# Optimization experiments

Hardware: AMD Instinct MI355X
Metric: run time of the kernel (lower is better)

## Reference

```python
import jax, jax.numpy as jnp
import numpy as np
from jax import lax
from jax.scipy.special import logsumexp

B, T, N = 256, 512, 128


def setup_inputs() -> dict:
    key = jax.random.key(0)
    k1, k2, k3 = jax.random.split(key, 3)
    emissions = jax.random.normal(k1, (B, T, N), dtype=jnp.float32)
    tag_ids = jax.random.randint(k2, (B, T), 0, N, dtype=jnp.int64)
    mask = jnp.ones((B, T), dtype=jnp.int32)
    # learned transition matrix (glorot-uniform-ish init)
    limit = float(np.sqrt(6.0 / (N + N)))
    trans = jax.random.uniform(k3, (N, N), minval=-limit, maxval=limit, dtype=jnp.float32)
    return {"emissions": emissions, "tag_ids": tag_ids, "mask": mask, "trans": trans}


def _sequence_score(emissions, tag_ids, maskf, trans):
    # unary: emission score of the gold tag at each valid step
    unary = jnp.take_along_axis(emissions, tag_ids[:, :, None], axis=2)[..., 0]  # [B,T]
    unary = jnp.sum(unary * maskf, axis=1)
    # binary: transition score between consecutive gold tags
    binary = trans[tag_ids[:, :-1], tag_ids[:, 1:]] * maskf[:, 1:]  # [B,T-1]
    return unary + jnp.sum(binary, axis=1)


def _log_norm(emissions, maskf, trans):
    # forward algorithm over time via lax.scan; alpha: [B,N]
    alpha0 = emissions[:, 0]
    em = jnp.swapaxes(emissions, 0, 1)[1:]   # [T-1,B,N]
    mk = jnp.swapaxes(maskf, 0, 1)[1:]       # [T-1,B]

    def step(alpha, xs):
        emit_t, m_t = xs
        new = logsumexp(alpha[:, :, None] + trans[None], axis=1) + emit_t
        alpha = jnp.where(m_t[:, None] > 0, new, alpha)
        return alpha, None

    alpha, _ = lax.scan(step, alpha0, (em, mk))
    return logsumexp(alpha, axis=1)  # [B]


def _viterbi_decode(emissions, maskf, trans):
    alpha0 = emissions[:, 0]
    em = jnp.swapaxes(emissions, 0, 1)[1:]
    mk = jnp.swapaxes(maskf, 0, 1)[1:]
    idx = jnp.arange(N, dtype=jnp.int32)[None]

    def fwd(alpha, xs):
        emit_t, m_t = xs
        scores = alpha[:, :, None] + trans[None]        # [B,N,N]
        bp = jnp.argmax(scores, axis=1).astype(jnp.int32)  # [B,N]
        new = jnp.max(scores, axis=1) + emit_t
        valid = m_t[:, None] > 0
        alpha = jnp.where(valid, new, alpha)
        bp = jnp.where(valid, bp, idx)  # carry same tag through padding
        return alpha, bp

    alpha, bps = lax.scan(fwd, alpha0, (em, mk))  # bps: [T-1,B,N]
    last_tag = jnp.argmax(alpha, axis=1).astype(jnp.int32)  # [B]

    def bwd(tag, bp_t):
        new_tag = jnp.take_along_axis(bp_t, tag[:, None], axis=1)[:, 0]
        return new_tag, new_tag

    _, tags_rev = lax.scan(bwd, last_tag, bps[::-1])  # [T-1,B]
    tags = jnp.concatenate([tags_rev[::-1], last_tag[None]], axis=0)  # [T,B]
    return jnp.swapaxes(tags, 0, 1)  # [B,T]


def reference(emissions, tag_ids, mask, trans):
    maskf = mask.astype(emissions.dtype)
    log_likelihood = _sequence_score(emissions, tag_ids, maskf, trans) - _log_norm(emissions, maskf, trans)
    predict = _viterbi_decode(emissions, maskf, trans)
    return (log_likelihood, trans, predict)
```

## Files before the change

### kernel.cpp

```cpp
#include <hip/hip_runtime.h>
#include <cmath>

#define BB 256
#define TT 512
#define NN 128
#define LN2F 0.6931471805599453f

typedef __bf16 bf16x8 __attribute__((ext_vector_type(8)));
typedef float floatx4 __attribute__((ext_vector_type(4)));

__device__ __forceinline__ float wave_max64(float v) {
    #pragma unroll
    for (int off = 32; off; off >>= 1) v = fmaxf(v, __shfl_xor(v, off));
    return v;
}
__device__ __forceinline__ float wave_sum64(float v) {
    #pragma unroll
    for (int off = 32; off; off >>= 1) v += __shfl_xor(v, off);
    return v;
}
__device__ __forceinline__ int wave_argmax128(float v0, float v1, int l) {
    float m = fmaxf(v0, v1);
    float wm = wave_max64(m);
    unsigned long long ball = __ballot(m == wm);
    int lane = __ffsll(ball) - 1;
    int idx = (v0 == wm) ? (2 * l) : (2 * l + 1);
    return __shfl(idx, lane);
}

__device__ __forceinline__ __bf16 to_bf16(float f) {
    unsigned u = __float_as_uint(f);
    unsigned r = (u + 0x7FFFu + ((u >> 16) & 1u)) >> 16;
    union { unsigned short s; __bf16 b; } cv;
    cv.s = (unsigned short)r;
    return cv.b;
}

__device__ __forceinline__ int padidx(int i) { return 36 * (i >> 5) + (i & 31); }

__global__ __launch_bounds__(1024, 4) void fwd_kernel(
        const float* __restrict__ em, const int* __restrict__ mask,
        const float* __restrict__ trans, float* __restrict__ outp,
        float* __restrict__ lognorm) {
    const int b = blockIdx.x;
    const int tid = threadIdx.x;
    const int w = tid >> 6;
    const int l = tid & 63;
    const bool isV = (w < 8);
    const int j = (l & 15) + 16 * (w & 7);
    const int q = l >> 4;
    const int i0 = 32 * q;

    __shared__ __align__(16) float apad[2][144];
    __shared__ __align__(16) __bf16 sbf[2][NN];
    __shared__ unsigned char bp_lds[TT * NN];
    __shared__ unsigned char tags_lds[TT];
    __shared__ unsigned char map_lds[8 * NN];
    __shared__ int entry_sh[8];
    __shared__ int msk[TT];
    __shared__ float piv[2];
    __shared__ float sfin[NN];
    __shared__ int misc[2];

    if (tid < TT) msk[tid] = mask[b * TT + tid];

    const float* emb = em + (size_t)b * TT * NN;

    float C[32];
    bf16x8 Bf[4];
    if (isV) {
        const float* tc = trans + (size_t)i0 * NN + j;
        #pragma unroll
        for (int r = 0; r < 32; ++r) C[r] = tc[(size_t)r * NN];
    } else {
        #pragma unroll
        for (int kc = 0; kc < 4; ++kc) {
            #pragma unroll
            for (int jj = 0; jj < 8; ++jj) {
                int row = kc * 32 + q * 8 + jj;
                Bf[kc][jj] = to_bf16(__expf(trans[(size_t)row * NN + j]));
            }
        }
    }

    float st = 0.f;
    int kacc = 0;
    {
        float a0 = emb[j];
        if (isV) {
            st = a0;
            if (l < 16) apad[0][padidx(j)] = a0;
        } else {
            st = __expf(a0);
            if (l < 16) sbf[0][j] = to_bf16(st);
            if (w == 8 && l == 0) piv[0] = st;
        }
    }
    float e_next = emb[NN + j];
    __syncthreads();

    for (int t = 1; t < TT; ++t) {
        const float e_cur = e_next;
        if (t + 1 < TT) e_next = emb[(size_t)(t + 1) * NN + j];
        const int m = msk[t];
        const int p = (t - 1) & 1, qb = t & 1;

        if (isV) {
            const float4* ap = (const float4*)(apad[p] + 36 * q);
            float m0 = -INFINITY, m1 = -INFINITY, m2 = -INFINITY, m3 = -INFINITY;
            int u0 = 0, u1 = 0, u2 = 0, u3 = 0;
            #pragma unroll
            for (int u = 0; u < 8; ++u) {
                float4 v = ap[u];
                float c0 = v.x + C[4*u+0]; u0 = (c0 > m0) ? u : u0; m0 = fmaxf(m0, c0);
                float c1 = v.y + C[4*u+1]; u1 = (c1 > m1) ? u : u1; m1 = fmaxf(m1, c1);
                float c2 = v.z + C[4*u+2]; u2 = (c2 > m2) ? u : u2; m2 = fmaxf(m2, c2);
                float c3 = v.w + C[4*u+3]; u3 = (c3 > m3) ? u : u3; m3 = fmaxf(m3, c3);
            }
            float bv = m0; int bx = i0 + 4 * u0;
            { int id = i0 + 4*u1 + 1; if (m1 > bv || (m1 == bv && id < bx)) { bv = m1; bx = id; } }
            { int id = i0 + 4*u2 + 2; if (m2 > bv || (m2 == bv && id < bx)) { bv = m2; bx = id; } }
            { int id = i0 + 4*u3 + 3; if (m3 > bv || (m3 == bv && id < bx)) { bv = m3; bx = id; } }
            #pragma unroll
            for (int off = 16; off <= 32; off <<= 1) {
                float ov = __shfl_xor(bv, off);
                int oi = __shfl_xor(bx, off);
                if (ov > bv || (ov == bv && oi < bx)) { bv = ov; bx = oi; }
            }
            if (l < 16) {
                float an; int bp;
                if (m) { an = bv + e_cur; bp = bx; }
                else   { an = st;         bp = j;  }
                st = an;
                apad[qb][padidx(j)] = an;
                bp_lds[t * NN + j] = (unsigned char)bp;
            }
        } else {
            if (m) {
                const __bf16* sp = sbf[p];
                floatx4 acc = {0.f, 0.f, 0.f, 0.f};
                #pragma unroll
                for (int kc = 0; kc < 4; ++kc) {
                    bf16x8 a = *(const bf16x8*)(sp + kc * 32 + q * 8);
                    acc = __builtin_amdgcn_mfma_f32_16x16x32_bf16(a, Bf[kc], acc, 0, 0, 0);
                }
                float dot = acc[0];
                const float pv = piv[p];
                const int k = (int)(__float_as_uint(pv) >> 23) - 127;
                const float scale = __uint_as_float((unsigned)(127 - k) << 23);
                st = dot * scale * __expf(e_cur);
                if (w == 8 && l == 0) kacc += k;
            }
            if (l < 16) sbf[qb][j] = to_bf16(st);
            if (w == 8 && l == 0) piv[qb] = st;
        }
        __syncthreads();
    }

    if (!isV && l < 16) sfin[j] = st;
    if (w == 8 && l == 0) misc[1] = kacc;
    if (w == 0) {
        float a0 = apad[1][padidx(2 * l)], a1 = apad[1][padidx(2 * l + 1)];
        int tg = wave_argmax128(a0, a1, l);
        if (l == 0) { misc[0] = tg; tags_lds[TT - 1] = (unsigned char)tg; }
    }
    __syncthreads();

    const int lo = 64 * (w & 7) + 1;
    const int hi = ((w & 7) == 7) ? (TT - 1) : (64 * (w & 7) + 64);
    if (isV) {
        int tA = 2 * l, tB = 2 * l + 1;
        for (int t = hi; t >= lo; --t) {
            tA = bp_lds[t * NN + tA];
            tB = bp_lds[t * NN + tB];
        }
        map_lds[(w & 7) * NN + 2 * l]     = (unsigned char)tA;
        map_lds[(w & 7) * NN + 2 * l + 1] = (unsigned char)tB;
    } else if (w == 8) {
        float v = sfin[2 * l] + sfin[2 * l + 1];
        v = wave_sum64(v);
        if (l == 0) lognorm[b] = __logf(v) + (float)misc[1] * LN2F;
    }
    __syncthreads();
    if (tid == 0) {
        int e = misc[0];
        entry_sh[7] = e;
        for (int c = 7; c >= 1; --c) { e = map_lds[c * NN + e]; entry_sh[c - 1] = e; }
    }
    __syncthreads();
    if (isV && l == 0) {
        int tg = entry_sh[w];
        for (int t = hi; t >= lo; --t) {
            tg = bp_lds[t * NN + tg];
            tags_lds[t - 1] = (unsigned char)tg;
        }
    }
    __syncthreads();
    if (tid < TT) outp[(size_t)b * TT + tid] = (float)tags_lds[tid];
}

__global__ __launch_bounds__(128, 1) void score_kernel(
        const float* __restrict__ em, const int* __restrict__ tags,
        const int* __restrict__ mask, const float* __restrict__ trans,
        const float* __restrict__ lognorm, float* __restrict__ out_ll) {
    const int b = blockIdx.x;
    const int tid = threadIdx.x;
    float acc = 0.f;
    for (int t = tid; t < TT; t += 128) {
        int tg = tags[b * TT + t];
        float mf = (float)mask[b * TT + t];
        acc += em[((size_t)b * TT + t) * NN + tg] * mf;
        if (t >= 1) {
            int tp = tags[b * TT + t - 1];
            acc += trans[tp * NN + tg] * mf;
        }
    }
    acc = wave_sum64(acc);
    __shared__ float rs[2];
    if ((tid & 63) == 0) rs[tid >> 6] = acc;
    __syncthreads();
    if (tid == 0) out_ll[b] = (rs[0] + rs[1]) - lognorm[b];
}

__global__ void copy_trans_kernel(const float* __restrict__ trans,
                                  float* __restrict__ dst) {
    int i = blockIdx.x * 256 + threadIdx.x;
    if (i < NN * NN) dst[i] = trans[i];
}

extern "C" void kernel_launch(void* const* d_in, const int* in_sizes, int n_in,
                              void* d_out, int out_size, void* d_ws, size_t ws_size,
                              hipStream_t stream) {
    const float* em = (const float*)d_in[0];
    const int* tags = (const int*)d_in[1];
    const int* mask = (const int*)d_in[2];
    const float* trans = (const float*)d_in[3];

    float* out = (float*)d_out;
    float* out_ll = out;
    float* out_trans = out + BB;
    float* out_pred = out + BB + NN * NN;

    float* lognorm = (float*)d_ws;

    hipLaunchKernelGGL(fwd_kernel, dim3(BB), dim3(1024), 0, stream,
                       em, mask, trans, out_pred, lognorm);
    hipLaunchKernelGGL(copy_trans_kernel, dim3(64), dim3(256), 0, stream,
                       trans, out_trans);
    hipLaunchKernelGGL(score_kernel, dim3(BB), dim3(128), 0, stream,
                       em, tags, mask, trans, lognorm, out_ll);
}
```

Before: 587.1 us.

## Spread Viterbi max-plus step across all 16 waves, overlapping with MFMA forward

The Viterbi recurrence was computed by 8 waves, each lane reducing 32 predecessors. All 16 waves now take part, each lane reducing 16 predecessors with one extra shuffle stage, and a new padded LDS layout. The 8 waves doing the bf16 MFMA forward-algorithm step now also run a Viterbi slice, which shortens the serial critical path of each timestep. In exchange those waves carry more registers and more work per step, and the per-step barrier waits on the combined work.

Measured after the change: 688.4 us. +17.3%, slower.

```diff
diff --git a/kernel.cpp b/kernel.cpp
--- a/kernel.cpp
+++ b/kernel.cpp
@@ -36,7 +36,7 @@
     return cv.b;
 }
 
-__device__ __forceinline__ int padidx(int i) { return 36 * (i >> 5) + (i & 31); }
+__device__ __forceinline__ int pidx(int i) { return 20 * (i >> 4) + (i & 15); }
 
 __global__ __launch_bounds__(1024, 4) void fwd_kernel(
         const float* __restrict__ em, const int* __restrict__ mask,
@@ -46,12 +46,14 @@
     const int tid = threadIdx.x;
     const int w = tid >> 6;
     const int l = tid & 63;
-    const bool isV = (w < 8);
-    const int j = (l & 15) + 16 * (w & 7);
-    const int q = l >> 4;
-    const int i0 = 32 * q;
-
-    __shared__ __align__(16) float apad[2][144];
+    const int j = (l & 7) + 8 * w;
+    const int g = l >> 3;
+    const int i0 = 16 * g;
+    const bool isS = (w >= 8);
+    const int js = (l & 15) + 16 * (w & 7);
+    const int qs = l >> 4;
+
+    __shared__ __align__(16) float apad[2][160];
     __shared__ __align__(16) __bf16 sbf[2][NN];
     __shared__ unsigned char bp_lds[TT * NN];
     __shared__ unsigned char tags_lds[TT];
@@ -66,51 +68,57 @@
 
     const float* emb = em + (size_t)b * TT * NN;
 
-    float C[32];
-    bf16x8 Bf[4];
-    if (isV) {
+    float C[16];
+    {
         const float* tc = trans + (size_t)i0 * NN + j;
         #pragma unroll
-        for (int r = 0; r < 32; ++r) C[r] = tc[(size_t)r * NN];
-    } else {
+        for (int r = 0; r < 16; ++r) C[r] = tc[(size_t)r * NN];
+    }
+    bf16x8 Bf[4];
+    if (isS) {
         #pragma unroll
         for (int kc = 0; kc < 4; ++kc) {
             #pragma unroll
             for (int jj = 0; jj < 8; ++jj) {
-                int row = kc * 32 + q * 8 + jj;
-                Bf[kc][jj] = to_bf16(__expf(trans[(size_t)row * NN + j]));
+                int row = kc * 32 + qs * 8 + jj;
+                Bf[kc][jj] = to_bf16(__expf(trans[(size_t)row * NN + js]));
             }
         }
     }
 
     float st = 0.f;
+    float ss = 0.f;
     int kacc = 0;
     {
         float a0 = emb[j];
-        if (isV) {
-            st = a0;
-            if (l < 16) apad[0][padidx(j)] = a0;
-        } else {
-            st = __expf(a0);
-            if (l < 16) sbf[0][j] = to_bf16(st);
-            if (w == 8 && l == 0) piv[0] = st;
+        st = a0;
+        if (l < 8) apad[0][pidx(j)] = a0;
+        if (isS) {
+            ss = __expf(emb[js]);
+            if (l < 16) sbf[0][js] = to_bf16(ss);
+            if (w == 8 && l == 0) piv[0] = ss;
         }
     }
     float e_next = emb[NN + j];
+    float es_next = isS ? emb[NN + js] : 0.f;
     __syncthreads();
 
     for (int t = 1; t < TT; ++t) {
         const float e_cur = e_next;
-        if (t + 1 < TT) e_next = emb[(size_t)(t + 1) * NN + j];
+        const float es_cur = es_next;
+        if (t + 1 < TT) {
+            e_next = emb[(size_t)(t + 1) * NN + j];
+            if (isS) es_next = emb[(size_t)(t + 1) * NN + js];
+        }
         const int m = msk[t];
         const int p = (t - 1) & 1, qb = t & 1;
 
-        if (isV) {
-            const float4* ap = (const float4*)(apad[p] + 36 * q);
+        {
+            const float4* ap = (const float4*)(apad[p] + 20 * g);
             float m0 = -INFINITY, m1 = -INFINITY, m2 = -INFINITY, m3 = -INFINITY;
             int u0 = 0, u1 = 0, u2 = 0, u3 = 0;
             #pragma unroll
-            for (int u = 0; u < 8; ++u) {
+            for (int u = 0; u < 4; ++u) {
                 float4 v = ap[u];
                 float c0 = v.x + C[4*u+0]; u0 = (c0 > m0) ? u : u0; m0 = fmaxf(m0, c0);
                 float c1 = v.y + C[4*u+1]; u1 = (c1 > m1) ? u : u1; m1 = fmaxf(m1, c1);
@@ -122,45 +130,47 @@
             { int id = i0 + 4*u2 + 2; if (m2 > bv || (m2 == bv && id < bx)) { bv = m2; bx = id; } }
             { int id = i0 + 4*u3 + 3; if (m3 > bv || (m3 == bv && id < bx)) { bv = m3; bx = id; } }
             #pragma unroll
-            for (int off = 16; off <= 32; off <<= 1) {
+            for (int off = 8; off <= 32; off <<= 1) {
                 float ov = __shfl_xor(bv, off);
                 int oi = __shfl_xor(bx, off);
                 if (ov > bv || (ov == bv && oi < bx)) { bv = ov; bx = oi; }
             }
-            if (l < 16) {
+            if (l < 8) {
                 float an; int bp;
                 if (m) { an = bv + e_cur; bp = bx; }
                 else   { an = st;         bp = j;  }
                 st = an;
-                apad[qb][padidx(j)] = an;
+                apad[qb][pidx(j)] = an;
                 bp_lds[t * NN + j] = (unsigned char)bp;
             }
-        } else {
+        }
+
+        if (isS) {
             if (m) {
                 const __bf16* sp = sbf[p];
                 floatx4 acc = {0.f, 0.f, 0.f, 0.f};
                 #pragma unroll
                 for (int kc = 0; kc < 4; ++kc) {
-                    bf16x8 a = *(const bf16x8*)(sp + kc * 32 + q * 8);
+                    bf16x8 a = *(const bf16x8*)(sp + kc * 32 + qs * 8);
                     acc = __builtin_amdgcn_mfma_f32_16x16x32_bf16(a, Bf[kc], acc, 0, 0, 0);
                 }
                 float dot = acc[0];
                 const float pv = piv[p];
                 const int k = (int)(__float_as_uint(pv) >> 23) - 127;
                 const float scale = __uint_as_float((unsigned)(127 - k) << 23);
-                st = dot * scale * __expf(e_cur);
+                ss = dot * scale * __expf(es_cur);
                 if (w == 8 && l == 0) kacc += k;
             }
-            if (l < 16) sbf[qb][j] = to_bf16(st);
-            if (w == 8 && l == 0) piv[qb] = st;
+            if (l < 16) sbf[qb][js] = to_bf16(ss);
+            if (w == 8 && l == 0) piv[qb] = ss;
         }
         __syncthreads();
     }
 
-    if (!isV && l < 16) sfin[j] = st;
+    if (isS && l < 16) sfin[js] = ss;
     if (w == 8 && l == 0) misc[1] = kacc;
     if (w == 0) {
-        float a0 = apad[1][padidx(2 * l)], a1 = apad[1][padidx(2 * l + 1)];
+        float a0 = apad[1][pidx(2 * l)], a1 = apad[1][pidx(2 * l + 1)];
         int tg = wave_argmax128(a0, a1, l);
         if (l == 0) { misc[0] = tg; tags_lds[TT - 1] = (unsigned char)tg; }
     }
@@ -168,7 +178,7 @@
 
     const int lo = 64 * (w & 7) + 1;
     const int hi = ((w & 7) == 7) ? (TT - 1) : (64 * (w & 7) + 64);
-    if (isV) {
+    if (w < 8) {
         int tA = 2 * l, tB = 2 * l + 1;
         for (int t = hi; t >= lo; --t) {
             tA = bp_lds[t * NN + tA];
@@ -188,7 +198,7 @@
         for (int c = 7; c >= 1; --c) { e = map_lds[c * NN + e]; entry_sh[c - 1] = e; }
     }
     __syncthreads();
-    if (isV && l == 0) {
+    if (w < 8 && l == 0) {
         int tg = entry_sh[w];
         for (int t = hi; t >= lo; --t) {
             tg = bp_lds[t * NN + tg];
```

## Split Viterbi and forward-algorithm work into separate 512-thread blocks

Applied to the files above, without the earlier changes.

Each batch element was handled by one 1024-thread block with 8 Viterbi waves and 8 MFMA forward-algorithm waves sharing one barrier per step. Now the grid is doubled: blocks below BB run Viterbi, the rest run the log-normalizer, each with 512 threads and its own barriers. The Viterbi loop is also unrolled by two, ping-ponging between two fixed state buffers. The aim is to stop the two recurrences from waiting on each other at every step and to shrink barrier scope, at the cost of a second block per batch reloading emissions and mask, while each block still reserves the full shared-memory footprint.

After: 541.5 us. 7.8% less time.

```diff
diff --git a/kernel.cpp b/kernel.cpp
--- a/kernel.cpp
+++ b/kernel.cpp
@@ -38,20 +38,21 @@
 
 __device__ __forceinline__ int padidx(int i) { return 36 * (i >> 5) + (i & 31); }
 
-__global__ __launch_bounds__(1024, 4) void fwd_kernel(
+__global__ __launch_bounds__(512, 4) void fwd_kernel(
         const float* __restrict__ em, const int* __restrict__ mask,
         const float* __restrict__ trans, float* __restrict__ outp,
         float* __restrict__ lognorm) {
-    const int b = blockIdx.x;
+    const int bi = blockIdx.x;
+    const bool isV = bi < BB;
+    const int b = isV ? bi : bi - BB;
     const int tid = threadIdx.x;
     const int w = tid >> 6;
     const int l = tid & 63;
-    const bool isV = (w < 8);
-    const int j = (l & 15) + 16 * (w & 7);
+    const int j = (l & 15) + 16 * w;
     const int q = l >> 4;
     const int i0 = 32 * q;
 
-    __shared__ __align__(16) float apad[2][144];
+    __shared__ __align__(16) float stA[144], stB[144];
     __shared__ __align__(16) __bf16 sbf[2][NN];
     __shared__ unsigned char bp_lds[TT * NN];
     __shared__ unsigned char tags_lds[TT];
@@ -62,51 +63,33 @@
     __shared__ float sfin[NN];
     __shared__ int misc[2];
 
-    if (tid < TT) msk[tid] = mask[b * TT + tid];
+    msk[tid] = mask[b * TT + tid];
 
     const float* emb = em + (size_t)b * TT * NN;
 
-    float C[32];
-    bf16x8 Bf[4];
     if (isV) {
-        const float* tc = trans + (size_t)i0 * NN + j;
-        #pragma unroll
-        for (int r = 0; r < 32; ++r) C[r] = tc[(size_t)r * NN];
-    } else {
-        #pragma unroll
-        for (int kc = 0; kc < 4; ++kc) {
-            #pragma unroll
-            for (int jj = 0; jj < 8; ++jj) {
-                int row = kc * 32 + q * 8 + jj;
-                Bf[kc][jj] = to_bf16(__expf(trans[(size_t)row * NN + j]));
-            }
-        }
-    }
-
-    float st = 0.f;
-    int kacc = 0;
-    {
-        float a0 = emb[j];
-        if (isV) {
+        float C[32];
+        {
+            const float* tc = trans + (size_t)i0 * NN + j;
+            #pragma unroll
+            for (int r = 0; r < 32; ++r) C[r] = tc[(size_t)r * NN];
+        }
+        float st = 0.f;
+        {
+            float a0 = emb[j];
             st = a0;
-            if (l < 16) apad[0][padidx(j)] = a0;
-        } else {
-            st = __expf(a0);
-            if (l < 16) sbf[0][j] = to_bf16(st);
-            if (w == 8 && l == 0) piv[0] = st;
-        }
-    }
-    float e_next = emb[NN + j];
-    __syncthreads();
-
-    for (int t = 1; t < TT; ++t) {
-        const float e_cur = e_next;
-        if (t + 1 < TT) e_next = emb[(size_t)(t + 1) * NN + j];
-        const int m = msk[t];
-        const int p = (t - 1) & 1, qb = t & 1;
-
-        if (isV) {
-            const float4* ap = (const float4*)(apad[p] + 36 * q);
+            if (l < 16) stA[padidx(j)] = a0;
+        }
+        float e_next = emb[NN + j];
+        __syncthreads();
+
+        const float4* apA = (const float4*)(stA + 36 * q);
+        const float4* apB = (const float4*)(stB + 36 * q);
+
+        auto VSTEP = [&](int t, const float4* ap, float* dst) {
+            const float e_cur = e_next;
+            if (t + 1 < TT) e_next = emb[(size_t)(t + 1) * NN + j];
+            const int m = msk[t];
             float m0 = -INFINITY, m1 = -INFINITY, m2 = -INFINITY, m3 = -INFINITY;
             int u0 = 0, u1 = 0, u2 = 0, u3 = 0;
             #pragma unroll
@@ -132,10 +115,73 @@
                 if (m) { an = bv + e_cur; bp = bx; }
                 else   { an = st;         bp = j;  }
                 st = an;
-                apad[qb][padidx(j)] = an;
+                dst[padidx(j)] = an;
                 bp_lds[t * NN + j] = (unsigned char)bp;
             }
-        } else {
+            __syncthreads();
+        };
+
+        for (int t = 1; t < TT - 1; t += 2) {
+            VSTEP(t, apA, stB);
+            VSTEP(t + 1, apB, stA);
+        }
+        VSTEP(TT - 1, apA, stB);
+
+        if (w == 0) {
+            float a0 = stB[padidx(2 * l)], a1 = stB[padidx(2 * l + 1)];
+            int tg = wave_argmax128(a0, a1, l);
+            if (l == 0) { misc[0] = tg; tags_lds[TT - 1] = (unsigned char)tg; }
+        }
+        __syncthreads();
+        const int lo = 64 * w + 1;
+        const int hi = (w == 7) ? (TT - 1) : (64 * w + 64);
+        {
+            int tA = 2 * l, tB = 2 * l + 1;
+            for (int t = hi; t >= lo; --t) {
+                tA = bp_lds[t * NN + tA];
+                tB = bp_lds[t * NN + tB];
+            }
+            map_lds[w * NN + 2 * l]     = (unsigned char)tA;
+            map_lds[w * NN + 2 * l + 1] = (unsigned char)tB;
+        }
+        __syncthreads();
+        if (tid == 0) {
+            int e = misc[0];
+            entry_sh[7] = e;
+            for (int c = 7; c >= 1; --c) { e = map_lds[c * NN + e]; entry_sh[c - 1] = e; }
+        }
+        __syncthreads();
+        if (l == 0) {
+            int tg = entry_sh[w];
+            for (int t = hi; t >= lo; --t) {
+                tg = bp_lds[t * NN + tg];
+                tags_lds[t - 1] = (unsigned char)tg;
+            }
+        }
+        __syncthreads();
+        outp[(size_t)b * TT + tid] = (float)tags_lds[tid];
+    } else {
+        bf16x8 Bf[4];
+        #pragma unroll
+        for (int kc = 0; kc < 4; ++kc) {
+            #pragma unroll
+            for (int jj = 0; jj < 8; ++jj) {
+                int row = kc * 32 + q * 8 + jj;
+                Bf[kc][jj] = to_bf16(__expf(trans[(size_t)row * NN + j]));
+            }
+        }
+        float ss = __expf(emb[j]);
+        int kacc = 0;
+        if (l < 16) sbf[0][j] = to_bf16(ss);
+        if (tid == 0) piv[0] = ss;
+        float e_next = emb[NN + j];
+        __syncthreads();
+
+        for (int t = 1; t < TT; ++t) {
+            const float e_cur = e_next;
+            if (t + 1 < TT) e_next = emb[(size_t)(t + 1) * NN + j];
+            const int m = msk[t];
+            const int p = (t - 1) & 1, qb = t & 1;
             if (m) {
                 const __bf16* sp = sbf[p];
                 floatx4 acc = {0.f, 0.f, 0.f, 0.f};
@@ -148,55 +194,23 @@
                 const float pv = piv[p];
                 const int k = (int)(__float_as_uint(pv) >> 23) - 127;
                 const float scale = __uint_as_float((unsigned)(127 - k) << 23);
-                st = dot * scale * __expf(e_cur);
-                if (w == 8 && l == 0) kacc += k;
-            }
-            if (l < 16) sbf[qb][j] = to_bf16(st);
-            if (w == 8 && l == 0) piv[qb] = st;
-        }
-        __syncthreads();
+                ss = dot * scale * __expf(e_cur);
+                if (tid == 0) kacc += k;
+            }
+            if (l < 16) sbf[qb][j] = to_bf16(ss);
+            if (tid == 0) piv[qb] = ss;
+            __syncthreads();
+        }
+
+        if (l < 16) sfin[j] = ss;
+        if (tid == 0) misc[1] = kacc;
+        __syncthreads();
+        if (w == 0) {
+            float v = sfin[2 * l] + sfin[2 * l + 1];
+            v = wave_sum64(v);
+            if (l == 0) lognorm[b] = __logf(v) + (float)misc[1] * LN2F;
+        }
     }
-
-    if (!isV && l < 16) sfin[j] = st;
-    if (w == 8 && l == 0) misc[1] = kacc;
-    if (w == 0) {
-        float a0 = apad[1][padidx(2 * l)], a1 = apad[1][padidx(2 * l + 1)];
-        int tg = wave_argmax128(a0, a1, l);
-        if (l == 0) { misc[0] = tg; tags_lds[TT - 1] = (unsigned char)tg; }
-    }
-    __syncthreads();
-
-    const int lo = 64 * (w & 7) + 1;
-    const int hi = ((w & 7) == 7) ? (TT - 1) : (64 * (w & 7) + 64);
-    if (isV) {
-        int tA = 2 * l, tB = 2 * l + 1;
-        for (int t = hi; t >= lo; --t) {
-            tA = bp_lds[t * NN + tA];
-            tB = bp_lds[t * NN + tB];
-        }
-        map_lds[(w & 7) * NN + 2 * l]     = (unsigned char)tA;
-        map_lds[(w & 7) * NN + 2 * l + 1] = (unsigned char)tB;
-    } else if (w == 8) {
-        float v = sfin[2 * l] + sfin[2 * l + 1];
-        v = wave_sum64(v);
-        if (l == 0) lognorm[b] = __logf(v) + (float)misc[1] * LN2F;
-    }
-    __syncthreads();
-    if (tid == 0) {
-        int e = misc[0];
-        entry_sh[7] = e;
-        for (int c = 7; c >= 1; --c) { e = map_lds[c * NN + e]; entry_sh[c - 1] = e; }
-    }
-    __syncthreads();
-    if (isV && l == 0) {
-        int tg = entry_sh[w];
-        for (int t = hi; t >= lo; --t) {
-            tg = bp_lds[t * NN + tg];
-            tags_lds[t - 1] = (unsigned char)tg;
-        }
-    }
-    __syncthreads();
-    if (tid < TT) outp[(size_t)b * TT + tid] = (float)tags_lds[tid];
 }
 
 __global__ __launch_bounds__(128, 1) void score_kernel(
@@ -243,7 +257,7 @@
 
     float* lognorm = (float*)d_ws;
 
-    hipLaunchKernelGGL(fwd_kernel, dim3(BB), dim3(1024), 0, stream,
+    hipLaunchKernelGGL(fwd_kernel, dim3(2 * BB), dim3(512), 0, stream,
                        em, mask, trans, out_pred, lognorm);
     hipLaunchKernelGGL(copy_trans_kernel, dim3(64), dim3(256), 0, stream,
                        trans, out_trans);
```
